# Kernel tuning notes

Hardware: AMD Instinct MI355X
Metric: run time of the kernel (lower is better)

Reference implementation:

```python
import jax, jax.numpy as jnp
import numpy as np


def _softmax_bmm(sjt, x):
    # sjt: [b, m, n] scores; softmax over n, then weighted sum of x [b, n, d]
    a = jax.nn.softmax(sjt, axis=2)
    return jnp.einsum('bmn,bnd->bmd', a, x)


def concat_att(x, y, Wc1, Wc2, vc):
    s1 = x @ Wc1  # [b, n, h]
    s2 = y @ Wc2  # [b, m, h]
    sjt = jnp.tanh(s1[:, None, :, :] + s2[:, :, None, :]) @ vc  # [b, m, n]
    return _softmax_bmm(sjt, x)


def dot_att(x, y, Wd, vd):
    # torch: vd(tanh(Wd(x_n * y_m))) ; (x_n*y_m)@Wd == einsum over feature dim
    s = jnp.einsum('bnd,bmd,dh->bmnh', x, y, Wd)  # [b, m, n, h]
    sjt = jnp.tanh(s) @ vd  # [b, m, n]
    return _softmax_bmm(sjt, x)


def minus_att(x, y, Wm, vm):
    # (x_n - y_m)@Wm == x@Wm broadcast-minus y@Wm
    sx = x @ Wm  # [b, n, h]
    sy = y @ Wm  # [b, m, h]
    sjt = jnp.tanh(sx[:, None, :, :] - sy[:, :, None, :]) @ vm  # [b, m, n]
    return _softmax_bmm(sjt, x)


def bilinear_att(x, y, Wb):
    sjt = jnp.einsum('bmd,bnd->bmn', y, x @ Wb)
    return _softmax_bmm(sjt, x)


def setup_inputs() -> dict:
    H = 128          # hidden_size
    D = 2 * H        # encoder feature dim (2*hidden)
    B, N, M = 4, 256, 256
    key = jax.random.key(0)
    ks = jax.random.split(key, 12)
    sD = 1.0 / np.sqrt(D)
    sH = 1.0 / np.sqrt(H)
    return {
        'x0_enc': jax.random.normal(ks[0], (B, N, D), jnp.float32),
        'x1_enc': jax.random.normal(ks[1], (B, M, D), jnp.float32),
        'Wc1': jax.random.normal(ks[2], (D, H), jnp.float32) * sD,
        'Wc2': jax.random.normal(ks[3], (D, H), jnp.float32) * sD,
        'vc': jax.random.normal(ks[4], (H,), jnp.float32) * sH,
        'Wb': jax.random.normal(ks[5], (D, D), jnp.float32) * sD,
        'Wd1': jax.random.normal(ks[6], (D, H), jnp.float32) * sD,
        'vd1': jax.random.normal(ks[7], (H,), jnp.float32) * sH,
        'Wd2': jax.random.normal(ks[8], (D, H), jnp.float32) * sD,
        'vd2': jax.random.normal(ks[9], (H,), jnp.float32) * sH,
        'Wm': jax.random.normal(ks[10], (D, H), jnp.float32) * sD,
        'vm': jax.random.normal(ks[11], (H,), jnp.float32) * sH,
    }


def reference(x0_enc, x1_enc, Wc1, Wc2, vc, Wb, Wd1, vd1, Wd2, vd2, Wm, vm):
    # attention_type == 'all'
    qtc = concat_att(x0_enc, x1_enc, Wc1, Wc2, vc)   # [b, m, d]
    qtb = bilinear_att(x0_enc, x1_enc, Wb)           # [b, m, d]
    qts = dot_att(x0_enc, x1_enc, Wd1, vd1)          # [b, m, d]
    qtd = dot_att(x1_enc, x0_enc, Wd2, vd2)          # [b, n, d] (n == m)
    qtm = minus_att(x0_enc, x1_enc, Wm, vm)          # [b, m, d]
    stacked = jnp.stack([x1_enc, qts, qtc, qtd, qtb, qtm], axis=0)
    return jnp.max(stacked, axis=0)
```

## Files before the change

kernel.cpp:

```cpp
#include <hip/hip_runtime.h>
#include <math.h>

typedef short short8 __attribute__((ext_vector_type(8)));
typedef float f32x4 __attribute__((ext_vector_type(4)));
typedef unsigned short US;

#if __has_builtin(__builtin_amdgcn_exp2f)
#define EXP2(x) __builtin_amdgcn_exp2f(x)
#else
#define EXP2(x) exp2f(x)
#endif
#define RCP(x) __builtin_amdgcn_rcpf(x)

#define C2 2.8853900817779268f

__device__ __forceinline__ float bf2f(US u) {
    return __uint_as_float(((unsigned int)u) << 16);
}
__device__ __forceinline__ US f2bf(float f) {
    unsigned int x = __float_as_uint(f);
    return (US)((x + 0x7FFFu + ((x >> 16) & 1u)) >> 16);
}
__device__ __forceinline__ US f2bf_fast(float f) {
    return (US)((__float_as_uint(f) + 0x8000u) >> 16);
}


__global__ void prep_gemm_kernel(const float* __restrict__ x0, const float* __restrict__ x1,
                                 const float* __restrict__ Wc1, const float* __restrict__ Wc2,
                                 const float* __restrict__ Wm, const float* __restrict__ Wd1,
                                 const float* __restrict__ Wd2, const float* __restrict__ Wb,
                                 US* __restrict__ x0b, US* __restrict__ x1b,
                                 US* __restrict__ x0lo, US* __restrict__ x1lo,
                                 US* __restrict__ WdT1, US* __restrict__ WdT2,
                                 US* __restrict__ x0T, US* __restrict__ x1T,
                                 US* __restrict__ S1T, US* __restrict__ SXT,
                                 float* __restrict__ S2, float* __restrict__ SY,
                                 US* __restrict__ XBhi, US* __restrict__ XBlo) {
    const int id = blockIdx.x;
    const int t = threadIdx.x;
    if (id < 512) {
        const int tensor = id >> 8;
        const float* src = tensor ? x1 : x0;
        US* dhi = tensor ? x1b : x0b;
        US* dlo = tensor ? x1lo : x0lo;
        const int idx = (id & 255) * 256 + t;
        float4 v = ((const float4*)src)[idx];
        float f[4] = {v.x, v.y, v.z, v.w};
        ushort4 hi, lo;
        US* hp = (US*)&hi;
        US* lp = (US*)&lo;
        #pragma unroll
        for (int j = 0; j < 4; ++j) {
            US h = f2bf(f[j]);
            hp[j] = h;
            lp[j] = f2bf(f[j] - bf2f(h));
        }
        ((ushort4*)dhi)[idx] = hi;
        ((ushort4*)dlo)[idx] = lo;
        return;
    }
    if (id < 768) {
        const int j = id - 512;
        const int mat = j >> 7;
        const float* src = mat ? Wd2 : Wd1;
        US* dst = mat ? WdT2 : WdT1;
        const int el = (j & 127) * 256 + t;
        const int d = el >> 7, h = el & 127;
        dst[h * 256 + d] = f2bf(src[d * 128 + h]);
        return;
    }
    if (id < 1792) {
        const int j = id - 768;
        const int tensor = j >> 9;
        const int j2 = j & 511;
        const int b = j2 >> 7;
        const int dp = j2 & 127;
        const float* src = tensor ? x1 : x0;
        US* dst = tensor ? x1T : x0T;
        float2 v = *(const float2*)(src + (size_t)(b * 256 + t) * 256 + dp * 2);
        dst[(size_t)(b * 256 + dp * 2) * 256 + t] = f2bf(v.x);
        dst[(size_t)(b * 256 + dp * 2 + 1) * 256 + t] = f2bf(v.y);
        return;
    }
    const int gid = id - 1792;
    const int rg = gid & 15;
    const int t2 = gid >> 4;
    const int b = t2 / 3;
    const int which = t2 - b * 3;
    const int lane = t & 63;
    const int w = t >> 6;
    const int arow = lane & 15;
    const int kgrp = lane >> 4;

    const float* Araw = ((which == 2) ? x1 : x0) + (size_t)(b * 256 + rg * 16 + arow) * 256 + kgrp * 8;

    const f32x4 vzero = {0.f, 0.f, 0.f, 0.f};
    f32x4 acc[4];
    #pragma unroll
    for (int cj = 0; cj < 4; ++cj) acc[cj] = vzero;

    if (which == 1) {
        #pragma unroll
        for (int kk = 0; kk < 8; ++kk) {
            float4 a0 = *(const float4*)(Araw + kk * 32);
            float4 a1 = *(const float4*)(Araw + kk * 32 + 4);
            float af[8] = {a0.x, a0.y, a0.z, a0.w, a1.x, a1.y, a1.z, a1.w};
            short8 ahi, alo;
            #pragma unroll
            for (int j = 0; j < 8; ++j) {
                US h = f2bf(af[j]);
                ahi[j] = (short)h;
                alo[j] = (short)f2bf(af[j] - bf2f(h));
            }
            #pragma unroll
            for (int cj = 0; cj < 4; ++cj) {
                const int ct = w * 4 + cj;
                const int dp = ct * 16 + arow;
                short8 bhi, blo;
                #pragma unroll
                for (int j = 0; j < 8; ++j) {
                    float wv = Wb[(size_t)(kk * 32 + kgrp * 8 + j) * 256 + dp];
                    US h = f2bf(wv);
                    bhi[j] = (short)h;
                    blo[j] = (short)f2bf(wv - bf2f(h));
                }
                acc[cj] = __builtin_amdgcn_mfma_f32_16x16x32_bf16(ahi, bhi, acc[cj], 0, 0, 0);
                acc[cj] = __builtin_amdgcn_mfma_f32_16x16x32_bf16(ahi, blo, acc[cj], 0, 0, 0);
                acc[cj] = __builtin_amdgcn_mfma_f32_16x16x32_bf16(alo, bhi, acc[cj], 0, 0, 0);
            }
        }
        #pragma unroll
        for (int cj = 0; cj < 4; ++cj) {
            const int ct = w * 4 + cj;
            #pragma unroll
            for (int r = 0; r < 4; ++r) {
                const int n = rg * 16 + kgrp * 4 + r;
                const int dp = ct * 16 + arow;
                float val = acc[cj][r];
                US h = f2bf(val);
                US l = f2bf(val - bf2f(h));
                XBhi[(size_t)(b * 256 + n) * 256 + dp] = h;
                XBlo[(size_t)(b * 256 + n) * 256 + dp] = l;
            }
        }
    } else {
        #pragma unroll
        for (int kk = 0; kk < 8; ++kk) {
            float4 a0 = *(const float4*)(Araw + kk * 32);
            float4 a1 = *(const float4*)(Araw + kk * 32 + 4);
            float af[8] = {a0.x, a0.y, a0.z, a0.w, a1.x, a1.y, a1.z, a1.w};
            short8 a;
            #pragma unroll
            for (int j = 0; j < 8; ++j) a[j] = (short)f2bf(af[j]);
            #pragma unroll
            for (int cj = 0; cj < 4; ++cj) {
                const int ct = w * 4 + cj;
                const int h = (ct < 8) ? ct * 16 + arow : (ct - 8) * 16 + arow;
                const float* Wsrc = (ct < 8) ? ((which == 0) ? Wc1 : Wc2) : Wm;
                short8 bf;
                #pragma unroll
                for (int j = 0; j < 8; ++j)
                    bf[j] = (short)f2bf(Wsrc[(size_t)(kk * 32 + kgrp * 8 + j) * 128 + h]);
                acc[cj] = __builtin_amdgcn_mfma_f32_16x16x32_bf16(a, bf, acc[cj], 0, 0, 0);
            }
        }
        #pragma unroll
        for (int cj = 0; cj < 4; ++cj) {
            const int ct = w * 4 + cj;
            #pragma unroll
            for (int r = 0; r < 4; ++r) {
                const int row = rg * 16 + kgrp * 4 + r;
                const int h = (ct < 8) ? ct * 16 + arow : (ct - 8) * 16 + arow;
                float val = acc[cj][r];
                if (which == 0) {
                    US* dst = (ct < 8) ? S1T : SXT;
                    dst[(size_t)(b * 256 + row) * 128 + h] = f2bf(val);
                } else {
                    float* dst = (ct < 8) ? S2 : SY;
                    dst[(size_t)(b * 256 + row) * 128 + h] = val;
                }
            }
        }
    }
}

__global__ __launch_bounds__(512, 4)
void combo_kernel(const US* __restrict__ x0b, const US* __restrict__ x1b,
                  const US* __restrict__ x1lo,
                  const US* __restrict__ WdT1, const US* __restrict__ WdT2,
                  const float* __restrict__ x0, const float* __restrict__ x1,
                  const float* __restrict__ vd1, const float* __restrict__ vd2,
                  const US* __restrict__ S1T, const US* __restrict__ SXT,
                  const float* __restrict__ S2, const float* __restrict__ SY,
                  const float* __restrict__ vc, const float* __restrict__ vm,
                  const US* __restrict__ XBhi, const US* __restrict__ XBlo,
                  float* __restrict__ sjt_s, float* __restrict__ sjt_d,
                  float* __restrict__ sjt_c, float* __restrict__ sjt_m,
                  float* __restrict__ sjt_b) {
    __shared__ __align__(16) US Wp[128 * 256];
    const int bid = blockIdx.x;
    const int t = threadIdx.x;
    const int lane = t & 63;
    const int w = t >> 6;
    const int arow = lane & 15;
    const int kgrp = lane >> 4;

    if (bid >= 3072) {
        const int idx = bid - 3072;
        const int b = idx >> 5;
        const int rem = idx & 31;
        const int mt = rem >> 2;
        const int nq = rem & 3;
        const int m0 = mt * 32 + (w & 1) * 16;
        const int nt = nq * 4 + (w >> 1);
        const size_t abase = (size_t)(b * 256 + m0 + arow) * 256 + kgrp * 8;
        const size_t bbase0 = (size_t)(b * 256 + nt * 16 + arow) * 256 + kgrp * 8;
        const f32x4 vzero = {0.f, 0.f, 0.f, 0.f};
        f32x4 acc = vzero;
        #pragma unroll
        for (int kk = 0; kk < 8; ++kk) {
            short8 ahi = *(const short8*)(x1b + abase + kk * 32);
            short8 alo = *(const short8*)(x1lo + abase + kk * 32);
            short8 bhi = *(const short8*)(XBhi + bbase0 + kk * 32);
            short8 blo = *(const short8*)(XBlo + bbase0 + kk * 32);
            acc = __builtin_amdgcn_mfma_f32_16x16x32_bf16(ahi, bhi, acc, 0, 0, 0);
            acc = __builtin_amdgcn_mfma_f32_16x16x32_bf16(ahi, blo, acc, 0, 0, 0);
            acc = __builtin_amdgcn_mfma_f32_16x16x32_bf16(alo, bhi, acc, 0, 0, 0);
        }
        float* outb = sjt_b + (size_t)b * 65536;
        #pragma unroll
        for (int r = 0; r < 4; ++r)
            outb[(size_t)(m0 + kgrp * 4 + r) * 256 + nt * 16 + arow] = acc[r];
        return;
    }

    const int q = bid / 3;
    const int r3 = bid - q * 3;

    if (r3 == 2) {
        const int b = q >> 8, m = q & 255;
        float* s2c  = (float*)Wp;
        float* sycN = s2c + 128;
        float* vc2l = sycN + 128;
        float* vm2l = vc2l + 128;
        float* vsums = vm2l + 128;

        if (t < 128) {
            s2c[t] = S2[(size_t)(b * 256 + m) * 128 + t] * C2;
            vc2l[t] = -2.0f * vc[t];
        } else if (t < 256) {
            const int h = t - 128;
            sycN[h] = -SY[(size_t)(b * 256 + m) * 128 + h] * C2;
            vm2l[h] = -2.0f * vm[h];
        } else if (t < 320) {
            const int l = t - 256;
            float sv = vc[l] + vc[l + 64];
            #pragma unroll
            for (int off = 32; off >= 1; off >>= 1) sv += __shfl_xor(sv, off);
            if (l == 0) vsums[0] = sv;
        } else if (t < 384) {
            const int l = t - 320;
            float sv = vm[l] + vm[l + 64];
            #pragma unroll
            for (int off = 32; off >= 1; off >>= 1) sv += __shfl_xor(sv, off);
            if (l == 0) vsums[1] = sv;
        }
        __syncthreads();

        const int half = t >> 8;
        const int n = t & 255;
        const US* sp = (half == 0 ? S1T : SXT) + (size_t)(b * 256 + n) * 128;
        const float* scoef = half == 0 ? s2c : sycN;
        const float* vco = half == 0 ? vc2l : vm2l;
        float accv = 0.f;
        #pragma unroll 2
        for (int hb = 0; hb < 16; ++hb) {
            short8 v8 = *(const short8*)(sp + hb * 8);
            #pragma unroll
            for (int j = 0; j < 8; ++j) {
                const int h = hb * 8 + j;
                float a = fmaf(bf2f((US)v8[j]), C2, scoef[h]);
                accv = fmaf(vco[h], RCP(EXP2(a) + 1.0f), accv);
            }
        }
        float* dst = half == 0 ? sjt_c : sjt_m;
        dst[(size_t)(b * 256 + m) * 256 + n] = accv + vsums[half];
        return;
    }

    const int idx = q * 2 + r3;
    const int m    = idx & 255;
    const int b    = (idx >> 8) & 3;
    const int mech = idx >> 10;
    const US* xA = (mech == 0 ? x0b : x1b) + (size_t)b * 65536;
    const float* yrow = (mech == 0 ? x1 : x0) + (size_t)(b * 256 + m) * 256;
    const US* WT = (mech == 0 ? WdT1 : WdT2);
    const float* v = (mech == 0 ? vd1 : vd2);
    float* out = (mech == 0 ? sjt_s : sjt_d) + (size_t)(b * 256 + m) * 256;

    {
        const int dslot = t & 31;
        const int hset = t >> 5;
        float yv[8];
        float4 y0 = *(const float4*)(yrow + dslot * 8);
        float4 y1 = *(const float4*)(yrow + dslot * 8 + 4);
        yv[0] = y0.x * C2; yv[1] = y0.y * C2; yv[2] = y0.z * C2; yv[3] = y0.w * C2;
        yv[4] = y1.x * C2; yv[5] = y1.y * C2; yv[6] = y1.z * C2; yv[7] = y1.w * C2;
        #pragma unroll
        for (int k = 0; k < 8; ++k) {
            const int hq = hset * 8 + k;
            short8 wv = *(const short8*)(WT + (size_t)hq * 256 + dslot * 8);
            short8 ov;
            #pragma unroll
            for (int j = 0; j < 8; ++j)
                ov[j] = (short)f2bf_fast(bf2f((US)wv[j]) * yv[j]);
            *(short8*)(&Wp[hq * 256 + ((dslot ^ (hq & 15)) << 3)]) = ov;
        }
    }
    __syncthreads();

    float v2[8], vsum = 0.f;
    #pragma unroll
    for (int j = 0; j < 8; ++j) {
        const float vvv = v[j * 16 + arow];
        vsum += vvv;
        v2[j] = -2.0f * vvv;
    }

    const f32x4 vzero = {0.f, 0.f, 0.f, 0.f};
    f32x4 acc[2][8];
    #pragma unroll
    for (int i = 0; i < 2; ++i)
        #pragma unroll
        for (int j = 0; j < 8; ++j) acc[i][j] = vzero;

    __builtin_amdgcn_s_setprio(1);
    #pragma unroll
    for (int kk = 0; kk < 8; ++kk) {
        short8 af[2];
        #pragma unroll
        for (int i = 0; i < 2; ++i)
            af[i] = *(const short8*)(xA + (size_t)(w * 32 + i * 16 + arow) * 256 + kk * 32 + kgrp * 8);
        const int sl = ((kk * 4 + kgrp) ^ arow) << 3;
        #pragma unroll
        for (int j = 0; j < 8; ++j) {
            short8 bfr = *(const short8*)(&Wp[(j * 16 + arow) * 256 + sl]);
            #pragma unroll
            for (int i = 0; i < 2; ++i)
                acc[i][j] = __builtin_amdgcn_mfma_f32_16x16x32_bf16(af[i], bfr, acc[i][j], 0, 0, 0);
        }
    }
    __builtin_amdgcn_s_setprio(0);

    float pacc[2][4];
    #pragma unroll
    for (int i = 0; i < 2; ++i)
        #pragma unroll
        for (int r = 0; r < 4; ++r) pacc[i][r] = 0.f;
    #pragma unroll
    for (int j = 0; j < 8; ++j)
        #pragma unroll
        for (int i = 0; i < 2; ++i)
            #pragma unroll
            for (int r = 0; r < 4; ++r)
                pacc[i][r] = fmaf(v2[j], RCP(EXP2(acc[i][j][r]) + 1.0f), pacc[i][r]);

    #pragma unroll
    for (int i = 0; i < 2; ++i)
        #pragma unroll
        for (int r = 0; r < 4; ++r) {
            float pp = pacc[i][r] + vsum;
            pp += __shfl_xor(pp, 1);
            pp += __shfl_xor(pp, 2);
            pp += __shfl_xor(pp, 4);
            pp += __shfl_xor(pp, 8);
            if (arow == 0) out[w * 32 + i * 16 + kgrp * 4 + r] = pp;
        }
}

__global__ void final_probs_kernel(const float* __restrict__ sjt_c, const float* __restrict__ sjt_m,
                                   const float* __restrict__ sjt_b,
                                   const float* __restrict__ sjt_s, const float* __restrict__ sjt_d,
                                   US* __restrict__ P) {
    __shared__ float srow[5][256];
    const int id = blockIdx.x;
    const int b = id >> 8, m = id & 255;
    const int t = threadIdx.x;
    const size_t bm = (size_t)(b * 256 + m) * 256;

    srow[0][t] = sjt_c[bm + t];
    srow[1][t] = sjt_m[bm + t];
    srow[2][t] = sjt_b[bm + t];
    srow[3][t] = sjt_s[bm + t];
    srow[4][t] = sjt_d[bm + t];
    __syncthreads();

    const int wv = t >> 6, lane = t & 63;
    for (int r = wv; r < 5; r += 4) {
        float v0 = srow[r][lane], v1 = srow[r][lane + 64];
        float v2 = srow[r][lane + 128], v3 = srow[r][lane + 192];
        float mx = fmaxf(fmaxf(v0, v1), fmaxf(v2, v3));
        #pragma unroll
        for (int off = 32; off >= 1; off >>= 1) mx = fmaxf(mx, __shfl_xor(mx, off));
        v0 = __expf(v0 - mx); v1 = __expf(v1 - mx);
        v2 = __expf(v2 - mx); v3 = __expf(v3 - mx);
        float s = v0 + v1 + v2 + v3;
        #pragma unroll
        for (int off = 32; off >= 1; off >>= 1) s += __shfl_xor(s, off);
        float inv = __fdividef(1.0f, s);
        srow[r][lane] = v0 * inv;       srow[r][lane + 64] = v1 * inv;
        srow[r][lane + 128] = v2 * inv; srow[r][lane + 192] = v3 * inv;
    }
    __syncthreads();

    #pragma unroll
    for (int r = 0; r < 5; ++r)
        P[(size_t)r * 262144 + bm + t] = f2bf(srow[r][t]);
}

__global__ __launch_bounds__(256)
void apply_kernel(const US* __restrict__ P, const US* __restrict__ x0T,
                  const US* __restrict__ x1T, const float* __restrict__ x1,
                  float* __restrict__ outp) {
    const int id = blockIdx.x;
    const int b = id >> 6;
    const int rem = id & 63;
    const int dt = rem >> 2;
    const int mq = rem & 3;
    const int t = threadIdx.x;
    const int lane = t & 63;
    const int w = t >> 6;
    const int arow = lane & 15;
    const int kgrp = lane >> 4;
    const int m0 = mq * 64 + w * 16;

    float vmax[4];
    #pragma unroll
    for (int r = 0; r < 4; ++r)
        vmax[r] = x1[(size_t)(b * 256 + m0 + kgrp * 4 + r) * 256 + dt * 16 + arow];

    const f32x4 vzero = {0.f, 0.f, 0.f, 0.f};
    #pragma unroll
    for (int mech = 0; mech < 5; ++mech) {
        const US* Bsrc = (mech == 4 ? x1T : x0T) + (size_t)(b * 256 + dt * 16 + arow) * 256;
        const US* Pm = P + (size_t)mech * 262144 + (size_t)(b * 256 + m0 + arow) * 256;
        f32x4 acc = vzero;
        #pragma unroll
        for (int kk = 0; kk < 8; ++kk) {
            short8 bf = *(const short8*)(Bsrc + kk * 32 + kgrp * 8);
            short8 af = *(const short8*)(Pm + kk * 32 + kgrp * 8);
            acc = __builtin_amdgcn_mfma_f32_16x16x32_bf16(af, bf, acc, 0, 0, 0);
        }
        #pragma unroll
        for (int r = 0; r < 4; ++r)
            vmax[r] = fmaxf(vmax[r], acc[r]);
    }

    #pragma unroll
    for (int r = 0; r < 4; ++r)
        outp[(size_t)(b * 256 + m0 + kgrp * 4 + r) * 256 + dt * 16 + arow] = vmax[r];
}

extern "C" void kernel_launch(void* const* d_in, const int* in_sizes, int n_in,
                              void* d_out, int out_size, void* d_ws, size_t ws_size,
                              hipStream_t stream) {
    (void)in_sizes; (void)n_in; (void)out_size; (void)ws_size;
    const float* x0  = (const float*)d_in[0];
    const float* x1  = (const float*)d_in[1];
    const float* Wc1 = (const float*)d_in[2];
    const float* Wc2 = (const float*)d_in[3];
    const float* vc  = (const float*)d_in[4];
    const float* Wb  = (const float*)d_in[5];
    const float* Wd1 = (const float*)d_in[6];
    const float* vd1 = (const float*)d_in[7];
    const float* Wd2 = (const float*)d_in[8];
    const float* vd2 = (const float*)d_in[9];
    const float* Wm  = (const float*)d_in[10];
    const float* vm  = (const float*)d_in[11];

    char* ws = (char*)d_ws;
    US*    x0b    = (US*)(ws + 0);
    US*    x1b    = (US*)(ws + 524288);
    US*    x0lo   = (US*)(ws + 1048576);
    US*    x1lo   = (US*)(ws + 1572864);
    US*    WdT1   = (US*)(ws + 2097152);
    US*    WdT2   = (US*)(ws + 2162688);
    US*    S1T    = (US*)(ws + 2228224);
    US*    SXT    = (US*)(ws + 2490368);
    float* S2     = (float*)(ws + 2752512);
    float* SY     = (float*)(ws + 3276800);
    US*    XBhi   = (US*)(ws + 3801088);
    US*    XBlo   = (US*)(ws + 4325376);
    US*    x0T    = (US*)(ws + 4849664);
    US*    x1T    = (US*)(ws + 5373952);
    float* sjt_b  = (float*)(ws + 5898240);
    float* sjt_s  = (float*)(ws + 6946816);
    float* sjt_d  = (float*)(ws + 7995392);
    float* sjt_c  = (float*)(ws + 9043968);
    float* sjt_m  = (float*)(ws + 10092544);
    US*    P      = (US*)(ws + 11141120);

    prep_gemm_kernel<<<1984, 256, 0, stream>>>(x0, x1, Wc1, Wc2, Wm, Wd1, Wd2, Wb,
                                               x0b, x1b, x0lo, x1lo, WdT1, WdT2,
                                               x0T, x1T, S1T, SXT, S2, SY, XBhi, XBlo);
    combo_kernel<<<3200, 512, 0, stream>>>(x0b, x1b, x1lo, WdT1, WdT2, x0, x1, vd1, vd2,
                                           S1T, SXT, S2, SY, vc, vm, XBhi, XBlo,
                                           sjt_s, sjt_d, sjt_c, sjt_m, sjt_b);
    final_probs_kernel<<<1024, 256, 0, stream>>>(sjt_c, sjt_m, sjt_b, sjt_s, sjt_d, P);
    apply_kernel<<<256, 256, 0, stream>>>(P, x0T, x1T, x1, (float*)d_out);
}
```

Measured before the change: 102.0 us.

## Move concat/minus score computation from combo kernel into softmax kernel

The concat and minus attention score rows were computed by dedicated blocks inside combo_kernel and written to global memory, then re-read by the softmax kernel. They are now computed directly inside final_probs_kernel, which grows to 512 threads and keeps those scores in shared memory. This drops the sjt_c/sjt_m global round trip and shrinks combo_kernel's grid. The cost is a heavier softmax kernel with 1024 blocks doing the tanh loops, which may overlap less well with the MFMA work than before.

```diff
diff --git a/kernel.cpp b/kernel.cpp
--- a/kernel.cpp
+++ b/kernel.cpp
@@ -191,12 +191,8 @@
                   const US* __restrict__ WdT1, const US* __restrict__ WdT2,
                   const float* __restrict__ x0, const float* __restrict__ x1,
                   const float* __restrict__ vd1, const float* __restrict__ vd2,
-                  const US* __restrict__ S1T, const US* __restrict__ SXT,
-                  const float* __restrict__ S2, const float* __restrict__ SY,
-                  const float* __restrict__ vc, const float* __restrict__ vm,
                   const US* __restrict__ XBhi, const US* __restrict__ XBlo,
                   float* __restrict__ sjt_s, float* __restrict__ sjt_d,
-                  float* __restrict__ sjt_c, float* __restrict__ sjt_m,
                   float* __restrict__ sjt_b) {
     __shared__ __align__(16) US Wp[128 * 256];
     const int bid = blockIdx.x;
@@ -206,8 +202,8 @@
     const int arow = lane & 15;
     const int kgrp = lane >> 4;
 
-    if (bid >= 3072) {
-        const int idx = bid - 3072;
+    if (bid >= 2048) {
+        const int idx = bid - 2048;
         const int b = idx >> 5;
         const int rem = idx & 31;
         const int mt = rem >> 2;
@@ -235,39 +231,139 @@
         return;
     }
 
-    const int q = bid / 3;
-    const int r3 = bid - q * 3;
-
-    if (r3 == 2) {
-        const int b = q >> 8, m = q & 255;
-        float* s2c  = (float*)Wp;
-        float* sycN = s2c + 128;
-        float* vc2l = sycN + 128;
-        float* vm2l = vc2l + 128;
-        float* vsums = vm2l + 128;
-
-        if (t < 128) {
-            s2c[t] = S2[(size_t)(b * 256 + m) * 128 + t] * C2;
-            vc2l[t] = -2.0f * vc[t];
-        } else if (t < 256) {
-            const int h = t - 128;
-            sycN[h] = -SY[(size_t)(b * 256 + m) * 128 + h] * C2;
-            vm2l[h] = -2.0f * vm[h];
-        } else if (t < 320) {
-            const int l = t - 256;
-            float sv = vc[l] + vc[l + 64];
-            #pragma unroll
-            for (int off = 32; off >= 1; off >>= 1) sv += __shfl_xor(sv, off);
-            if (l == 0) vsums[0] = sv;
-        } else if (t < 384) {
-            const int l = t - 320;
-            float sv = vm[l] + vm[l + 64];
-            #pragma unroll
-            for (int off = 32; off >= 1; off >>= 1) sv += __shfl_xor(sv, off);
-            if (l == 0) vsums[1] = sv;
-        }
-        __syncthreads();
-
+    const int id2 = bid;
+    const int m    = id2 & 255;
+    const int b    = (id2 >> 8) & 3;
+    const int mech = id2 >> 10;
+    const US* xA = (mech == 0 ? x0b : x1b) + (size_t)b * 65536;
+    const float* yrow = (mech == 0 ? x1 : x0) + (size_t)(b * 256 + m) * 256;
+    const US* WT = (mech == 0 ? WdT1 : WdT2);
+    const float* v = (mech == 0 ? vd1 : vd2);
+    float* out = (mech == 0 ? sjt_s : sjt_d) + (size_t)(b * 256 + m) * 256;
+
+    {
+        const int dslot = t & 31;
+        const int hset = t >> 5;
+        float yv[8];
+        float4 y0 = *(const float4*)(yrow + dslot * 8);
+        float4 y1 = *(const float4*)(yrow + dslot * 8 + 4);
+        yv[0] = y0.x * C2; yv[1] = y0.y * C2; yv[2] = y0.z * C2; yv[3] = y0.w * C2;
+        yv[4] = y1.x * C2; yv[5] = y1.y * C2; yv[6] = y1.z * C2; yv[7] = y1.w * C2;
+        #pragma unroll
+        for (int k = 0; k < 8; ++k) {
+            const int hq = hset * 8 + k;
+            short8 wv = *(const short8*)(WT + (size_t)hq * 256 + dslot * 8);
+            short8 ov;
+            #pragma unroll
+            for (int j = 0; j < 8; ++j)
+                ov[j] = (short)f2bf_fast(bf2f((US)wv[j]) * yv[j]);
+            *(short8*)(&Wp[hq * 256 + ((dslot ^ (hq & 15)) << 3)]) = ov;
+        }
+    }
+    __syncthreads();
+
+    float v2[8], vsum = 0.f;
+    #pragma unroll
+    for (int j = 0; j < 8; ++j) {
+        const float vvv = v[j * 16 + arow];
+        vsum += vvv;
+        v2[j] = -2.0f * vvv;
+    }
+
+    const f32x4 vzero = {0.f, 0.f, 0.f, 0.f};
+    f32x4 acc[2][8];
+    #pragma unroll
+    for (int i = 0; i < 2; ++i)
+        #pragma unroll
+        for (int j = 0; j < 8; ++j) acc[i][j] = vzero;
+
+    __builtin_amdgcn_s_setprio(1);
+    #pragma unroll
+    for (int kk = 0; kk < 8; ++kk) {
+        short8 af[2];
+        #pragma unroll
+        for (int i = 0; i < 2; ++i)
+            af[i] = *(const short8*)(xA + (size_t)(w * 32 + i * 16 + arow) * 256 + kk * 32 + kgrp * 8);
+        const int sl = ((kk * 4 + kgrp) ^ arow) << 3;
+        #pragma unroll
+        for (int j = 0; j < 8; ++j) {
+            short8 bfr = *(const short8*)(&Wp[(j * 16 + arow) * 256 + sl]);
+            #pragma unroll
+            for (int i = 0; i < 2; ++i)
+                acc[i][j] = __builtin_amdgcn_mfma_f32_16x16x32_bf16(af[i], bfr, acc[i][j], 0, 0, 0);
+        }
+    }
+    __builtin_amdgcn_s_setprio(0);
+
+    float pacc[2][4];
+    #pragma unroll
+    for (int i = 0; i < 2; ++i)
+        #pragma unroll
+        for (int r = 0; r < 4; ++r) pacc[i][r] = 0.f;
+    #pragma unroll
+    for (int j = 0; j < 8; ++j)
+        #pragma unroll
+        for (int i = 0; i < 2; ++i)
+            #pragma unroll
+            for (int r = 0; r < 4; ++r)
+                pacc[i][r] = fmaf(v2[j], RCP(EXP2(acc[i][j][r]) + 1.0f), pacc[i][r]);
+
+    #pragma unroll
+    for (int i = 0; i < 2; ++i)
+        #pragma unroll
+        for (int r = 0; r < 4; ++r) {
+            float pp = pacc[i][r] + vsum;
+            pp += __shfl_xor(pp, 1);
+            pp += __shfl_xor(pp, 2);
+            pp += __shfl_xor(pp, 4);
+            pp += __shfl_xor(pp, 8);
+            if (arow == 0) out[w * 32 + i * 16 + kgrp * 4 + r] = pp;
+        }
+}
+
+__global__ __launch_bounds__(512)
+void final_probs_kernel(const US* __restrict__ S1T, const US* __restrict__ SXT,
+                        const float* __restrict__ S2, const float* __restrict__ SY,
+                        const float* __restrict__ vc, const float* __restrict__ vm,
+                        const float* __restrict__ sjt_b,
+                        const float* __restrict__ sjt_s, const float* __restrict__ sjt_d,
+                        US* __restrict__ P) {
+    __shared__ float srow[5][256];
+    __shared__ float s2c[128], sycN[128], vc2l[128], vm2l[128];
+    __shared__ float vsums[2];
+    const int id = blockIdx.x;
+    const int b = id >> 8, m = id & 255;
+    const int t = threadIdx.x;
+    const size_t bm = (size_t)(b * 256 + m) * 256;
+
+    if (t < 128) {
+        s2c[t] = S2[(size_t)(b * 256 + m) * 128 + t] * C2;
+        vc2l[t] = -2.0f * vc[t];
+    } else if (t < 256) {
+        const int h = t - 128;
+        sycN[h] = -SY[(size_t)(b * 256 + m) * 128 + h] * C2;
+        vm2l[h] = -2.0f * vm[h];
+    } else if (t < 320) {
+        const int l = t - 256;
+        float sv = vc[l] + vc[l + 64];
+        #pragma unroll
+        for (int off = 32; off >= 1; off >>= 1) sv += __shfl_xor(sv, off);
+        if (l == 0) vsums[0] = sv;
+    } else if (t < 384) {
+        const int l = t - 320;
+        float sv = vm[l] + vm[l + 64];
+        #pragma unroll
+        for (int off = 32; off >= 1; off >>= 1) sv += __shfl_xor(sv, off);
+        if (l == 0) vsums[1] = sv;
+    }
+    {
+        const int n = t & 255;
+        if (t < 512) srow[2 + (t >> 8)][n] = (t < 256 ? sjt_b : sjt_s)[bm + n];
+        if (t < 256) srow[4][t] = sjt_d[bm + t];
+    }
+    __syncthreads();
+
+    {
         const int half = t >> 8;
         const int n = t & 255;
         const US* sp = (half == 0 ? S1T : SXT) + (size_t)(b * 256 + n) * 128;
@@ -284,120 +380,12 @@
                 accv = fmaf(vco[h], RCP(EXP2(a) + 1.0f), accv);
             }
         }
-        float* dst = half == 0 ? sjt_c : sjt_m;
-        dst[(size_t)(b * 256 + m) * 256 + n] = accv + vsums[half];
-        return;
-    }
-
-    const int idx = q * 2 + r3;
-    const int m    = idx & 255;
-    const int b    = (idx >> 8) & 3;
-    const int mech = idx >> 10;
-    const US* xA = (mech == 0 ? x0b : x1b) + (size_t)b * 65536;
-    const float* yrow = (mech == 0 ? x1 : x0) + (size_t)(b * 256 + m) * 256;
-    const US* WT = (mech == 0 ? WdT1 : WdT2);
-    const float* v = (mech == 0 ? vd1 : vd2);
-    float* out = (mech == 0 ? sjt_s : sjt_d) + (size_t)(b * 256 + m) * 256;
-
-    {
-        const int dslot = t & 31;
-        const int hset = t >> 5;
-        float yv[8];
-        float4 y0 = *(const float4*)(yrow + dslot * 8);
-        float4 y1 = *(const float4*)(yrow + dslot * 8 + 4);
-        yv[0] = y0.x * C2; yv[1] = y0.y * C2; yv[2] = y0.z * C2; yv[3] = y0.w * C2;
-        yv[4] = y1.x * C2; yv[5] = y1.y * C2; yv[6] = y1.z * C2; yv[7] = y1.w * C2;
-        #pragma unroll
-        for (int k = 0; k < 8; ++k) {
-            const int hq = hset * 8 + k;
-            short8 wv = *(const short8*)(WT + (size_t)hq * 256 + dslot * 8);
-            short8 ov;
-            #pragma unroll
-            for (int j = 0; j < 8; ++j)
-                ov[j] = (short)f2bf_fast(bf2f((US)wv[j]) * yv[j]);
-            *(short8*)(&Wp[hq * 256 + ((dslot ^ (hq & 15)) << 3)]) = ov;
-        }
+        srow[half][n] = accv + vsums[half];
     }
     __syncthreads();
 
-    float v2[8], vsum = 0.f;
-    #pragma unroll
-    for (int j = 0; j < 8; ++j) {
-        const float vvv = v[j * 16 + arow];
-        vsum += vvv;
-        v2[j] = -2.0f * vvv;
-    }
-
-    const f32x4 vzero = {0.f, 0.f, 0.f, 0.f};
-    f32x4 acc[2][8];
-    #pragma unroll
-    for (int i = 0; i < 2; ++i)
-        #pragma unroll
-        for (int j = 0; j < 8; ++j) acc[i][j] = vzero;
-
-    __builtin_amdgcn_s_setprio(1);
-    #pragma unroll
-    for (int kk = 0; kk < 8; ++kk) {
-        short8 af[2];
-        #pragma unroll
-        for (int i = 0; i < 2; ++i)
-            af[i] = *(const short8*)(xA + (size_t)(w * 32 + i * 16 + arow) * 256 + kk * 32 + kgrp * 8);
-        const int sl = ((kk * 4 + kgrp) ^ arow) << 3;
-        #pragma unroll
-        for (int j = 0; j < 8; ++j) {
-            short8 bfr = *(const short8*)(&Wp[(j * 16 + arow) * 256 + sl]);
-            #pragma unroll
-            for (int i = 0; i < 2; ++i)
-                acc[i][j] = __builtin_amdgcn_mfma_f32_16x16x32_bf16(af[i], bfr, acc[i][j], 0, 0, 0);
-        }
-    }
-    __builtin_amdgcn_s_setprio(0);
-
-    float pacc[2][4];
-    #pragma unroll
-    for (int i = 0; i < 2; ++i)
-        #pragma unroll
-        for (int r = 0; r < 4; ++r) pacc[i][r] = 0.f;
-    #pragma unroll
-    for (int j = 0; j < 8; ++j)
-        #pragma unroll
-        for (int i = 0; i < 2; ++i)
-            #pragma unroll
-            for (int r = 0; r < 4; ++r)
-                pacc[i][r] = fmaf(v2[j], RCP(EXP2(acc[i][j][r]) + 1.0f), pacc[i][r]);
-
-    #pragma unroll
-    for (int i = 0; i < 2; ++i)
-        #pragma unroll
-        for (int r = 0; r < 4; ++r) {
-            float pp = pacc[i][r] + vsum;
-            pp += __shfl_xor(pp, 1);
-            pp += __shfl_xor(pp, 2);
-            pp += __shfl_xor(pp, 4);
-            pp += __shfl_xor(pp, 8);
-            if (arow == 0) out[w * 32 + i * 16 + kgrp * 4 + r] = pp;
-        }
-}
-
-__global__ void final_probs_kernel(const float* __restrict__ sjt_c, const float* __restrict__ sjt_m,
-                                   const float* __restrict__ sjt_b,
-                                   const float* __restrict__ sjt_s, const float* __restrict__ sjt_d,
-                                   US* __restrict__ P) {
-    __shared__ float srow[5][256];
-    const int id = blockIdx.x;
-    const int b = id >> 8, m = id & 255;
-    const int t = threadIdx.x;
-    const size_t bm = (size_t)(b * 256 + m) * 256;
-
-    srow[0][t] = sjt_c[bm + t];
-    srow[1][t] = sjt_m[bm + t];
-    srow[2][t] = sjt_b[bm + t];
-    srow[3][t] = sjt_s[bm + t];
-    srow[4][t] = sjt_d[bm + t];
-    __syncthreads();
-
     const int wv = t >> 6, lane = t & 63;
-    for (int r = wv; r < 5; r += 4) {
+    for (int r = wv; r < 5; r += 8) {
         float v0 = srow[r][lane], v1 = srow[r][lane + 64];
         float v2 = srow[r][lane + 128], v3 = srow[r][lane + 192];
         float mx = fmaxf(fmaxf(v0, v1), fmaxf(v2, v3));
@@ -414,9 +402,11 @@
     }
     __syncthreads();
 
-    #pragma unroll
-    for (int r = 0; r < 5; ++r)
-        P[(size_t)r * 262144 + bm + t] = f2bf(srow[r][t]);
+    for (int idx = t; idx < 1280; idx += 512) {
+        const int r = idx >> 8;
+        const int n = idx & 255;
+        P[(size_t)r * 262144 + bm + n] = f2bf(srow[r][n]);
+    }
 }
 
 __global__ __launch_bounds__(256)
@@ -497,16 +487,14 @@
     float* sjt_b  = (float*)(ws + 5898240);
     float* sjt_s  = (float*)(ws + 6946816);
     float* sjt_d  = (float*)(ws + 7995392);
-    float* sjt_c  = (float*)(ws + 9043968);
-    float* sjt_m  = (float*)(ws + 10092544);
-    US*    P      = (US*)(ws + 11141120);
+    US*    P      = (US*)(ws + 9043968);
 
     prep_gemm_kernel<<<1984, 256, 0, stream>>>(x0, x1, Wc1, Wc2, Wm, Wd1, Wd2, Wb,
                                                x0b, x1b, x0lo, x1lo, WdT1, WdT2,
                                                x0T, x1T, S1T, SXT, S2, SY, XBhi, XBlo);
-    combo_kernel<<<3200, 512, 0, stream>>>(x0b, x1b, x1lo, WdT1, WdT2, x0, x1, vd1, vd2,
-                                           S1T, SXT, S2, SY, vc, vm, XBhi, XBlo,
-                                           sjt_s, sjt_d, sjt_c, sjt_m, sjt_b);
-    final_probs_kernel<<<1024, 256, 0, stream>>>(sjt_c, sjt_m, sjt_b, sjt_s, sjt_d, P);
+    combo_kernel<<<2176, 512, 0, stream>>>(x0b, x1b, x1lo, WdT1, WdT2, x0, x1, vd1, vd2,
+                                           XBhi, XBlo, sjt_s, sjt_d, sjt_b);
+    final_probs_kernel<<<1024, 512, 0, stream>>>(S1T, SXT, S2, SY, vc, vm, sjt_b,
+                                                 sjt_s, sjt_d, P);
     apply_kernel<<<256, 256, 0, stream>>>(P, x0T, x1T, x1, (float*)d_out);
 }
```

After: 100.4 us. About the same (-1.5%).
